# Kernel optimization log

Measured on AMD Instinct MI355X. Metric: run time of the kernel, lower is better.

The kernel has to match this reference:

```python
import jax, jax.numpy as jnp
import numpy as np

ALPHA = 0.2   # LeakyReLU slope from source
HEADS = 8

def _proj(x, W, s, b):
    # Conv3D(kernel=1, no bias) + fused inference BatchNorm affine + LeakyReLU
    y = jnp.einsum('nchwd,de->nchwe', x, W) * s + b
    return jnp.where(y >= 0, y, ALPHA * y)

def setup_inputs() -> dict:
    key = jax.random.key(0)
    ks = jax.random.split(key, 13)
    N, D, H, W, C = 2, 64, 64, 64, 64   # D == in_channels (axis 1), C is last axis
    KC, VC = 64, 64
    p = lambda k, sh, sc=0.1: jax.random.normal(k, sh, jnp.float32) * sc
    return {
        'x':  jax.random.normal(ks[0], (N, D, H, W, C), jnp.float32),
        'Wk': p(ks[1], (D, KC)), 'sk': 1.0 + p(ks[2], (KC,)), 'bk': p(ks[3], (KC,)),
        'Wq': p(ks[4], (D, KC)), 'sq': 1.0 + p(ks[5], (KC,)), 'bq': p(ks[6], (KC,)),
        'Wv': p(ks[7], (D, VC)), 'sv': 1.0 + p(ks[8], (VC,)), 'bv': p(ks[9], (VC,)),
        'Wr': p(ks[10], (VC, D)), 'sr': 1.0 + p(ks[11], (D,)), 'br': p(ks[12], (D,)),
    }

def reference(x, Wk, sk, bk, Wq, sq, bq, Wv, sv, bv, Wr, sr, br):
    n, d, h, w, c = x.shape
    xt = jnp.transpose(x, (0, 4, 2, 3, 1))            # (n, c, h, w, d)
    keys    = _proj(xt, Wk, sk, bk)                   # (n, c, h, w, KC)
    queries = _proj(xt, Wq, sq, bq)
    values  = _proj(xt, Wv, sv, bv)
    T = c * h * w
    KC, VC = Wk.shape[1], Wv.shape[1]
    hk, hv = KC // HEADS, VC // HEADS                 # hk == hv required by source math
    K = jax.nn.softmax(keys.reshape(n, T, HEADS, hk), axis=1)      # softmax over tokens
    Q = jax.nn.softmax(queries.reshape(n, T, HEADS, hk), axis=-1)  # softmax over head channels
    V = values.reshape(n, T, HEADS, hv)
    ctx = jnp.einsum('ntak,ntav->nakv', K, V)         # (n, heads, hk, hv) small context
    # source: tf.matmul(context, query^T) contracts ctx's hv with query's hk axis
    att = jnp.einsum('nakv,ntav->nakt', ctx, Q)       # (n, heads, hk, T)
    # faithful raw reshape per head (n, hk, T) -> (n, c, h, w, hv), heads concat last
    att = att.reshape(n, HEADS, c, h, w, hv)
    agg = jnp.transpose(att, (0, 2, 3, 4, 1, 5)).reshape(n, c, h, w, HEADS * hv)
    rep = _proj(agg, Wr, sr, br)                      # (n, c, h, w, d)
    return x + jnp.transpose(rep, (0, 4, 2, 3, 1))
```

## Files before the change

kernel.cpp:

```cpp
#include <hip/hip_runtime.h>

#define ALPHA 0.2f

typedef const __attribute__((address_space(1))) unsigned int gu32;
typedef __attribute__((address_space(3))) unsigned int lu32;

__device__ float g_part[8192 * 576];
__device__ float g_red[2 * 32 * 1024];
__device__ float g_ctx[1024];

__global__ __launch_bounds__(256) void k_kv(
    const float* __restrict__ x,
    const float* __restrict__ Wk, const float* __restrict__ sk, const float* __restrict__ bk,
    const float* __restrict__ Wv, const float* __restrict__ sv, const float* __restrict__ bv)
{
  __shared__ __align__(16) float sh[12288];
  float* xt = sh;
  float* WL = sh + 4096;

  const int tid = threadIdx.x;
  const int bid = blockIdx.x;
  const int n  = bid >> 12;
  const int hw = bid & 4095;

  const float* xrow = x + (size_t)n * 16777216u + (size_t)hw * 64u;

  #pragma unroll
  for (int i = 0; i < 4; ++i) {
    int idx = tid + i * 256;
    int d = idx >> 4, c4 = (idx & 15) * 4;
    __builtin_amdgcn_global_load_lds((gu32*)(xrow + (size_t)d * 262144u + c4),
                                     (lu32*)&xt[idx * 4], 16, 0, 0);
  }
  #pragma unroll
  for (int i = 0; i < 8; ++i) {
    int idx = tid + i * 256;
    int d = idx >> 5, e4 = (idx & 31) * 4;
    const float* src = (e4 < 64) ? (Wk + d * 64 + e4) : (Wv + d * 64 + e4 - 64);
    __builtin_amdgcn_global_load_lds((gu32*)src, (lu32*)&WL[idx * 4], 16, 0, 0);
  }

  const int tok0 = (tid & 15) * 4;
  const int eg   = tid >> 4;
  const int e0   = eg * 8;
  const bool isK = (eg < 8);
  const int  ec  = isK ? e0 : (e0 - 64);

  const float* sp = (isK ? sk : sv) + ec;
  const float* bp = (isK ? bk : bv) + ec;
  float s8[8], b8[8];
  *(float4*)&s8[0] = *(const float4*)(sp);
  *(float4*)&s8[4] = *(const float4*)(sp + 4);
  *(float4*)&b8[0] = *(const float4*)(bp);
  *(float4*)&b8[4] = *(const float4*)(bp + 4);

  __syncthreads();

  float acc[4][8];
  #pragma unroll
  for (int t = 0; t < 4; ++t)
    #pragma unroll
    for (int j = 0; j < 8; ++j) acc[t][j] = 0.f;

  #pragma unroll 4
  for (int d = 0; d < 64; ++d) {
    float4 xv = *(const float4*)&xt[d * 64 + tok0];
    float4 wa = *(const float4*)&WL[d * 128 + e0];
    float4 wb = *(const float4*)&WL[d * 128 + e0 + 4];
    float xr[4] = {xv.x, xv.y, xv.z, xv.w};
    float w[8]  = {wa.x, wa.y, wa.z, wa.w, wb.x, wb.y, wb.z, wb.w};
    #pragma unroll
    for (int t = 0; t < 4; ++t)
      #pragma unroll
      for (int j = 0; j < 8; ++j) acc[t][j] += xr[t] * w[j];
  }

  __syncthreads();

  float* eK = sh;
  float* vV = sh + 4352;
  float* dst = (isK ? eK : vV);
  #pragma unroll
  for (int t = 0; t < 4; ++t) {
    float y8[8];
    #pragma unroll
    for (int j = 0; j < 8; ++j) {
      float y = acc[t][j] * s8[j] + b8[j];
      y = (y >= 0.f) ? y : ALPHA * y;
      if (isK) y = __expf(fminf(y, 60.f));
      y8[j] = y;
    }
    *(float4*)&dst[(tok0 + t) * 68 + ec]     = *(float4*)&y8[0];
    *(float4*)&dst[(tok0 + t) * 68 + ec + 4] = *(float4*)&y8[4];
  }
  __syncthreads();

  {
    float* pE = sh + 8704;
    float* pS = sh + 8960;
    const int ch = tid & 63;
    const int tq = tid >> 6;
    const int a8 = ch & ~7;

    float E = 0.f;
    float S[8];
    #pragma unroll
    for (int v = 0; v < 8; ++v) S[v] = 0.f;
    for (int t = tq * 16; t < tq * 16 + 16; ++t) {
      float e = eK[t * 68 + ch];
      float4 v0 = *(const float4*)&vV[t * 68 + a8];
      float4 v1 = *(const float4*)&vV[t * 68 + a8 + 4];
      E += e;
      S[0] += e * v0.x; S[1] += e * v0.y; S[2] += e * v0.z; S[3] += e * v0.w;
      S[4] += e * v1.x; S[5] += e * v1.y; S[6] += e * v1.z; S[7] += e * v1.w;
    }
    pE[tq * 64 + ch] = E;
    #pragma unroll
    for (int v = 0; v < 8; ++v) pS[(tq * 64 + ch) * 8 + v] = S[v];
    __syncthreads();

    if (tid < 64) {
      float* gp = g_part + (size_t)bid * 576u;
      float E4 = pE[tid] + pE[64 + tid] + pE[128 + tid] + pE[192 + tid];
      gp[tid] = E4;
      #pragma unroll
      for (int v = 0; v < 8; ++v) {
        float S4 = pS[tid * 8 + v] + pS[(64 + tid) * 8 + v]
                 + pS[(128 + tid) * 8 + v] + pS[(192 + tid) * 8 + v];
        gp[64 + v * 64 + tid] = S4;
      }
    }
  }
}

__global__ __launch_bounds__(256) void k_red() {
  const int ob = blockIdx.x & 3;
  const int bc = blockIdx.x >> 2;
  const int i  = ob * 256 + threadIdx.x;
  const int n = i >> 9, ch = (i & 511) >> 3, v = i & 7;
  const float* base = g_part + ((size_t)n * 4096u + (size_t)bc * 128u) * 576u;
  float l = 0.f, S = 0.f;
  #pragma unroll 8
  for (int b = 0; b < 128; ++b) {
    l += base[(size_t)b * 576u + ch];
    S += base[(size_t)b * 576u + 64u + (size_t)v * 64u + ch];
  }
  g_red[bc * 1024 + i]         = l;
  g_red[32768 + bc * 1024 + i] = S;
}

__global__ __launch_bounds__(256) void k_ctx() {
  int i = blockIdx.x * 256 + threadIdx.x;
  if (i >= 1024) return;
  float l = 0.f, S = 0.f;
  #pragma unroll
  for (int r = 0; r < 32; ++r) {
    l += g_red[r * 1024 + i];
    S += g_red[32768 + r * 1024 + i];
  }
  float c = (l > 0.f) ? (S / l) : 0.f;
  if (!(__builtin_fabsf(c) < 1e30f)) c = 0.f;
  g_ctx[i] = c;
}

__global__ __launch_bounds__(256) void k_att(
    const float* __restrict__ x,
    const float* __restrict__ Wq, const float* __restrict__ sq, const float* __restrict__ bq,
    const float* __restrict__ Wr, const float* __restrict__ sr, const float* __restrict__ br,
    float* __restrict__ out)
{
  __shared__ __align__(16) float WqA[64 * 65];
  __shared__ __align__(16) float xw[64 * 64];
  __shared__ __align__(16) float qL[64 * 64];
  __shared__ __align__(16) float ctxL[64 * 12];
  __shared__ float srL[64], brL[64];

  const int tid = threadIdx.x;
  const int lin = blockIdx.x;

  const int xcd   = lin & 7;
  const int jc    = (lin >> 3) & 7;
  const int rest  = lin >> 6;
  const int combo = rest * 8 + xcd;
  const int n     = combo >> 9;
  const int hp_lo = (combo >> 6) & 7;
  const int wp    = combo & 63;
  const int hp    = jc * 8 + hp_lo;
  const int hwp   = hp * 64 + wp;

  const int h_t   = hp_lo * 8 + (wp >> 3);
  const int wbase = (wp & 7) * 8;

  #pragma unroll
  for (int i = 0; i < 4; ++i) {
    int idx = tid + i * 256;
    __builtin_amdgcn_global_load_lds((gu32*)(Wq + idx * 4),
                                     (lu32*)&WqA[idx * 4], 16, 0, 0);
  }
  if (tid < 64) { srL[tid] = sr[tid]; brL[tid] = br[tid]; }

  for (int i = tid; i < 512; i += 256) {
    int ch = i >> 3, v = i & 7;
    ctxL[ch * 12 + v] = g_ctx[n * 512 + ch * 8 + v];
  }

  {
    const size_t xb = (size_t)n * 16777216u + (size_t)h_t * 4096u;
    #pragma unroll
    for (int i = 0; i < 16; ++i) {
      int idx = tid + i * 256;
      int d = idx >> 6, tok = idx & 63;
      int vpp = tok >> 3, cl = tok & 7;
      xw[d * 64 + tok] = x[xb + (size_t)d * 262144u + (size_t)(wbase + vpp) * 64u + (cl * 8 + jc)];
    }
  }
  __syncthreads();

  {
    const int tok0 = (tid & 31) * 2;
    const int ch0  = (tid >> 5) * 8;
    float acc0[8], acc1[8];
    #pragma unroll
    for (int j = 0; j < 8; ++j) { acc0[j] = 0.f; acc1[j] = 0.f; }
    #pragma unroll 4
    for (int d = 0; d < 64; ++d) {
      float2 xv = *(const float2*)&xw[d * 64 + tok0];
      float4 wa = *(const float4*)&WqA[d * 64 + ch0];
      float4 wb = *(const float4*)&WqA[d * 64 + ch0 + 4];
      float w[8] = {wa.x, wa.y, wa.z, wa.w, wb.x, wb.y, wb.z, wb.w};
      #pragma unroll
      for (int j = 0; j < 8; ++j) { acc0[j] += xv.x * w[j]; acc1[j] += xv.y * w[j]; }
    }
    float sv8[8], bv8[8];
    *(float4*)&sv8[0] = *(const float4*)(sq + ch0);
    *(float4*)&sv8[4] = *(const float4*)(sq + ch0 + 4);
    *(float4*)&bv8[0] = *(const float4*)(bq + ch0);
    *(float4*)&bv8[4] = *(const float4*)(bq + ch0 + 4);
    #pragma unroll
    for (int i = 0; i < 2; ++i) {
      float* a = (i == 0) ? acc0 : acc1;
      float mx = -3.0e38f;
      #pragma unroll
      for (int j = 0; j < 8; ++j) {
        float y = a[j] * sv8[j] + bv8[j];
        y = (y >= 0.f) ? y : ALPHA * y;
        a[j] = y;
        mx = fmaxf(mx, y);
      }
      float sum = 0.f;
      #pragma unroll
      for (int j = 0; j < 8; ++j) { a[j] = __expf(a[j] - mx); sum += a[j]; }
      float inv = 1.f / sum;
      float o8[8];
      #pragma unroll
      for (int j = 0; j < 8; ++j) o8[j] = a[j] * inv;
      const int t = tok0 + i;
      const int rot = (4 * t) & 63;
      *(float4*)&qL[t * 64 + ((ch0 + rot) & 63)]     = *(float4*)&o8[0];
      *(float4*)&qL[t * 64 + ((ch0 + 4 + rot) & 63)] = *(float4*)&o8[4];
    }
  }
  __syncthreads();

  #pragma unroll
  for (int i = 0; i < 4; ++i) {
    int idx = tid + i * 256;
    __builtin_amdgcn_global_load_lds((gu32*)(Wr + idx * 4),
                                     (lu32*)&xw[idx * 4], 16, 0, 0);
  }

  {
    float* aggL = WqA;
    const int cp = tid & 63, eb = tid >> 6;
    const int kk = cp >> 3, cl = cp & 7;
    #pragma unroll
    for (int je = 0; je < 16; ++je) {
      int e = eb * 16 + je;
      int a = e >> 3, vpp = e & 7;
      float4 c0 = *(const float4*)&ctxL[(a * 8 + kk) * 12];
      float4 c1 = *(const float4*)&ctxL[(a * 8 + kk) * 12 + 4];
      int t = vpp * 8 + cl;
      int rot = (4 * t) & 63;
      float4 q0 = *(const float4*)&qL[t * 64 + ((a * 8 + rot) & 63)];
      float4 q1 = *(const float4*)&qL[t * 64 + ((a * 8 + 4 + rot) & 63)];
      float s = q0.x * c0.x + q0.y * c0.y + q0.z * c0.z + q0.w * c0.w
              + q1.x * c1.x + q1.y * c1.y + q1.z * c1.z + q1.w * c1.w;
      aggL[cp * 65 + e] = s;
    }
  }
  __syncthreads();

  {
    const float* aggL = WqA;
    const int ci = tid & 63, dq = tid >> 6;
    float accr[16];
    #pragma unroll
    for (int i = 0; i < 16; ++i) accr[i] = 0.f;
    #pragma unroll 4
    for (int e = 0; e < 64; ++e) {
      float av = aggL[ci * 65 + e];
      const float* wr = &xw[e * 64 + dq * 16];
      #pragma unroll
      for (int i = 0; i < 16; ++i) accr[i] += av * wr[i];
    }
    const size_t xb = (size_t)n * 16777216u + (size_t)hwp * 64u + (size_t)ci;
    #pragma unroll
    for (int i = 0; i < 16; ++i) {
      int di = dq * 16 + i;
      float y = accr[i] * srL[di] + brL[di];
      y = (y >= 0.f) ? y : ALPHA * y;
      out[xb + (size_t)di * 262144u] = x[xb + (size_t)di * 262144u] + y;
    }
  }
}

extern "C" void kernel_launch(void* const* d_in, const int* in_sizes, int n_in,
                              void* d_out, int out_size, void* d_ws, size_t ws_size,
                              hipStream_t stream)
{
  (void)in_sizes; (void)n_in; (void)out_size; (void)d_ws; (void)ws_size;

  const float* x  = (const float*)d_in[0];
  const float* Wk = (const float*)d_in[1];
  const float* sk = (const float*)d_in[2];
  const float* bk = (const float*)d_in[3];
  const float* Wq = (const float*)d_in[4];
  const float* sq = (const float*)d_in[5];
  const float* bq = (const float*)d_in[6];
  const float* Wv = (const float*)d_in[7];
  const float* sv = (const float*)d_in[8];
  const float* bv = (const float*)d_in[9];
  const float* Wr = (const float*)d_in[10];
  const float* sr = (const float*)d_in[11];
  const float* br = (const float*)d_in[12];
  float* out = (float*)d_out;

  k_kv  <<<dim3(8192), dim3(256), 0, stream>>>(x, Wk, sk, bk, Wv, sv, bv);
  k_red <<<dim3(128),  dim3(256), 0, stream>>>();
  k_ctx <<<dim3(4),    dim3(256), 0, stream>>>();
  k_att <<<dim3(8192), dim3(256), 0, stream>>>(x, Wq, sq, bq, Wr, sr, br, out);
}
```

Before: 496.3 us.

## Restructure KV projection to wave-uniform weights and process two rows per block

The k_kv kernel now handles two hw rows per block, with half as many blocks. Each wave owns one 32-channel slice of K or V, so weight loads are wave-uniform reads straight from global memory, and x is read straight from global as float2 instead of staged through LDS. The reduction runs in two phases that write separate g_part slots, so the partial-sum layout seen by k_red stays the same. In k_att, the Wr weights are read from global with a wave-uniform index instead of being staged in LDS, and the agg tile uses padding of 68 so it can be written and read as float4. This trades LDS staging and its barriers for more global/scalar-cache traffic and higher register pressure from the 64-element accumulators.

Measured after the change: 523.4 us. 1.05x slower.

```diff
diff --git a/kernel.cpp b/kernel.cpp
--- a/kernel.cpp
+++ b/kernel.cpp
@@ -14,93 +14,79 @@
     const float* __restrict__ Wk, const float* __restrict__ sk, const float* __restrict__ bk,
     const float* __restrict__ Wv, const float* __restrict__ sv, const float* __restrict__ bv)
 {
-  __shared__ __align__(16) float sh[12288];
-  float* xt = sh;
-  float* WL = sh + 4096;
+  __shared__ __align__(16) float sh[11008];
+  float* eK = sh;
+  float* vV = sh + 4352;
+  float* pE = sh + 8704;
+  float* pS = sh + 8960;
 
   const int tid = threadIdx.x;
   const int bid = blockIdx.x;
-  const int n  = bid >> 12;
-  const int hw = bid & 4095;
-
-  const float* xrow = x + (size_t)n * 16777216u + (size_t)hw * 64u;
-
-  #pragma unroll
-  for (int i = 0; i < 4; ++i) {
-    int idx = tid + i * 256;
-    int d = idx >> 4, c4 = (idx & 15) * 4;
-    __builtin_amdgcn_global_load_lds((gu32*)(xrow + (size_t)d * 262144u + c4),
-                                     (lu32*)&xt[idx * 4], 16, 0, 0);
-  }
-  #pragma unroll
-  for (int i = 0; i < 8; ++i) {
-    int idx = tid + i * 256;
-    int d = idx >> 5, e4 = (idx & 31) * 4;
-    const float* src = (e4 < 64) ? (Wk + d * 64 + e4) : (Wv + d * 64 + e4 - 64);
-    __builtin_amdgcn_global_load_lds((gu32*)src, (lu32*)&WL[idx * 4], 16, 0, 0);
-  }
-
-  const int tok0 = (tid & 15) * 4;
-  const int eg   = tid >> 4;
-  const int e0   = eg * 8;
-  const bool isK = (eg < 8);
-  const int  ec  = isK ? e0 : (e0 - 64);
-
-  const float* sp = (isK ? sk : sv) + ec;
-  const float* bp = (isK ? bk : bv) + ec;
-  float s8[8], b8[8];
-  *(float4*)&s8[0] = *(const float4*)(sp);
-  *(float4*)&s8[4] = *(const float4*)(sp + 4);
-  *(float4*)&b8[0] = *(const float4*)(bp);
-  *(float4*)&b8[4] = *(const float4*)(bp + 4);
-
-  __syncthreads();
-
-  float acc[4][8];
-  #pragma unroll
-  for (int t = 0; t < 4; ++t)
-    #pragma unroll
-    for (int j = 0; j < 8; ++j) acc[t][j] = 0.f;
+  const int n   = bid >> 11;
+  const int hw0 = (bid & 2047) * 2;
+
+  const int pr  = tid & 63;
+  const int wv  = __builtin_amdgcn_readfirstlane(tid >> 6);
+  const bool isK = (wv < 2);
+  const int cbase = 32 * (wv & 1);
+  const float* Wsrc = (isK ? Wk : Wv) + cbase;
+  const float* sp   = (isK ? sk : sv) + cbase;
+  const float* bp   = (isK ? bk : bv) + cbase;
+
+  const float* xg = x + (size_t)n * 16777216u + (size_t)hw0 * 64u + 2 * pr;
+
+  float acc[2][32];
+  #pragma unroll
+  for (int t = 0; t < 2; ++t)
+    #pragma unroll
+    for (int c = 0; c < 32; ++c) acc[t][c] = 0.f;
 
   #pragma unroll 4
   for (int d = 0; d < 64; ++d) {
-    float4 xv = *(const float4*)&xt[d * 64 + tok0];
-    float4 wa = *(const float4*)&WL[d * 128 + e0];
-    float4 wb = *(const float4*)&WL[d * 128 + e0 + 4];
-    float xr[4] = {xv.x, xv.y, xv.z, xv.w};
-    float w[8]  = {wa.x, wa.y, wa.z, wa.w, wb.x, wb.y, wb.z, wb.w};
-    #pragma unroll
-    for (int t = 0; t < 4; ++t)
-      #pragma unroll
-      for (int j = 0; j < 8; ++j) acc[t][j] += xr[t] * w[j];
-  }
-
-  __syncthreads();
-
-  float* eK = sh;
-  float* vV = sh + 4352;
-  float* dst = (isK ? eK : vV);
-  #pragma unroll
-  for (int t = 0; t < 4; ++t) {
-    float y8[8];
-    #pragma unroll
-    for (int j = 0; j < 8; ++j) {
-      float y = acc[t][j] * s8[j] + b8[j];
-      y = (y >= 0.f) ? y : ALPHA * y;
-      if (isK) y = __expf(fminf(y, 60.f));
-      y8[j] = y;
-    }
-    *(float4*)&dst[(tok0 + t) * 68 + ec]     = *(float4*)&y8[0];
-    *(float4*)&dst[(tok0 + t) * 68 + ec + 4] = *(float4*)&y8[4];
-  }
-  __syncthreads();
-
-  {
-    float* pE = sh + 8704;
-    float* pS = sh + 8960;
-    const int ch = tid & 63;
-    const int tq = tid >> 6;
-    const int a8 = ch & ~7;
+    float2 xv = *(const float2*)(xg + (size_t)d * 262144u);
+    const float* wrow = Wsrc + d * 64;
+    #pragma unroll
+    for (int q = 0; q < 8; ++q) {
+      float4 w = *(const float4*)(wrow + q * 4);
+      acc[0][q*4+0] += xv.x * w.x; acc[0][q*4+1] += xv.x * w.y;
+      acc[0][q*4+2] += xv.x * w.z; acc[0][q*4+3] += xv.x * w.w;
+      acc[1][q*4+0] += xv.y * w.x; acc[1][q*4+1] += xv.y * w.y;
+      acc[1][q*4+2] += xv.y * w.z; acc[1][q*4+3] += xv.y * w.w;
+    }
+  }
+
+  #pragma unroll
+  for (int q = 0; q < 8; ++q) {
+    float4 s4 = *(const float4*)(sp + q * 4);
+    float4 b4 = *(const float4*)(bp + q * 4);
+    float ss[4] = {s4.x, s4.y, s4.z, s4.w};
+    float bb[4] = {b4.x, b4.y, b4.z, b4.w};
+    #pragma unroll
+    for (int j = 0; j < 4; ++j) {
+      #pragma unroll
+      for (int t = 0; t < 2; ++t) {
+        float y = acc[t][q*4+j] * ss[j] + bb[j];
+        y = (y >= 0.f) ? y : ALPHA * y;
+        if (isK) y = __expf(fminf(y, 60.f));
+        acc[t][q*4+j] = y;
+      }
+    }
+  }
+
+  const int prl = pr & 31;
+  float* dstbuf = isK ? eK : vV;
+  const int ch = tid & 63, tq = tid >> 6, a8 = ch & ~7;
+
+  #pragma unroll
+  for (int ph = 0; ph < 2; ++ph) {
+    if ((pr >> 5) == ph) {
+      #pragma unroll
+      for (int t = 0; t < 2; ++t)
+        #pragma unroll
+        for (int q = 0; q < 8; ++q)
+          *(float4*)&dstbuf[(prl*2 + t) * 68 + cbase + q*4] = *(float4*)&acc[t][q*4];
+    }
+    __syncthreads();
 
     float E = 0.f;
     float S[8];
@@ -120,7 +106,7 @@
     __syncthreads();
 
     if (tid < 64) {
-      float* gp = g_part + (size_t)bid * 576u;
+      float* gp = g_part + ((size_t)bid * 2u + ph) * 576u;
       float E4 = pE[tid] + pE[64 + tid] + pE[128 + tid] + pE[192 + tid];
       gp[tid] = E4;
       #pragma unroll
@@ -169,7 +155,7 @@
     const float* __restrict__ Wr, const float* __restrict__ sr, const float* __restrict__ br,
     float* __restrict__ out)
 {
-  __shared__ __align__(16) float WqA[64 * 65];
+  __shared__ __align__(16) float WqA[64 * 68];
   __shared__ __align__(16) float xw[64 * 64];
   __shared__ __align__(16) float qL[64 * 64];
   __shared__ __align__(16) float ctxL[64 * 12];
@@ -262,30 +248,28 @@
   }
   __syncthreads();
 
-  #pragma unroll
-  for (int i = 0; i < 4; ++i) {
-    int idx = tid + i * 256;
-    __builtin_amdgcn_global_load_lds((gu32*)(Wr + idx * 4),
-                                     (lu32*)&xw[idx * 4], 16, 0, 0);
-  }
-
   {
     float* aggL = WqA;
     const int cp = tid & 63, eb = tid >> 6;
     const int kk = cp >> 3, cl = cp & 7;
     #pragma unroll
-    for (int je = 0; je < 16; ++je) {
-      int e = eb * 16 + je;
-      int a = e >> 3, vpp = e & 7;
-      float4 c0 = *(const float4*)&ctxL[(a * 8 + kk) * 12];
-      float4 c1 = *(const float4*)&ctxL[(a * 8 + kk) * 12 + 4];
-      int t = vpp * 8 + cl;
-      int rot = (4 * t) & 63;
-      float4 q0 = *(const float4*)&qL[t * 64 + ((a * 8 + rot) & 63)];
-      float4 q1 = *(const float4*)&qL[t * 64 + ((a * 8 + 4 + rot) & 63)];
-      float s = q0.x * c0.x + q0.y * c0.y + q0.z * c0.z + q0.w * c0.w
-              + q1.x * c1.x + q1.y * c1.y + q1.z * c1.z + q1.w * c1.w;
-      aggL[cp * 65 + e] = s;
+    for (int j4 = 0; j4 < 4; ++j4) {
+      float s4[4];
+      #pragma unroll
+      for (int jj = 0; jj < 4; ++jj) {
+        int e = eb * 16 + j4 * 4 + jj;
+        int a = e >> 3, vpp = e & 7;
+        float4 c0 = *(const float4*)&ctxL[(a * 8 + kk) * 12];
+        float4 c1 = *(const float4*)&ctxL[(a * 8 + kk) * 12 + 4];
+        int t = vpp * 8 + cl;
+        int rot = (4 * t) & 63;
+        float4 q0 = *(const float4*)&qL[t * 64 + ((a * 8 + rot) & 63)];
+        float4 q1 = *(const float4*)&qL[t * 64 + ((a * 8 + 4 + rot) & 63)];
+        s4[jj] = q0.x * c0.x + q0.y * c0.y + q0.z * c0.z + q0.w * c0.w
+               + q1.x * c1.x + q1.y * c1.y + q1.z * c1.z + q1.w * c1.w;
+      }
+      *(float4*)&aggL[cp * 68 + eb * 16 + j4 * 4] =
+          make_float4(s4[0], s4[1], s4[2], s4[3]);
     }
   }
   __syncthreads();
@@ -293,15 +277,28 @@
   {
     const float* aggL = WqA;
     const int ci = tid & 63, dq = tid >> 6;
+    const int dqu = __builtin_amdgcn_readfirstlane(tid >> 6);
+    const float* WrU = Wr + dqu * 16;
     float accr[16];
     #pragma unroll
     for (int i = 0; i < 16; ++i) accr[i] = 0.f;
     #pragma unroll 4
-    for (int e = 0; e < 64; ++e) {
-      float av = aggL[ci * 65 + e];
-      const float* wr = &xw[e * 64 + dq * 16];
-      #pragma unroll
-      for (int i = 0; i < 16; ++i) accr[i] += av * wr[i];
+    for (int ec = 0; ec < 16; ++ec) {
+      float4 a4 = *(const float4*)&aggL[ci * 68 + ec * 4];
+      float av[4] = {a4.x, a4.y, a4.z, a4.w};
+      #pragma unroll
+      for (int j = 0; j < 4; ++j) {
+        const float* wrow = WrU + (ec * 4 + j) * 64;
+        float4 w0 = *(const float4*)(wrow);
+        float4 w1 = *(const float4*)(wrow + 4);
+        float4 w2 = *(const float4*)(wrow + 8);
+        float4 w3 = *(const float4*)(wrow + 12);
+        float aj = av[j];
+        accr[0]  += aj * w0.x; accr[1]  += aj * w0.y; accr[2]  += aj * w0.z; accr[3]  += aj * w0.w;
+        accr[4]  += aj * w1.x; accr[5]  += aj * w1.y; accr[6]  += aj * w1.z; accr[7]  += aj * w1.w;
+        accr[8]  += aj * w2.x; accr[9]  += aj * w2.y; accr[10] += aj * w2.z; accr[11] += aj * w2.w;
+        accr[12] += aj * w3.x; accr[13] += aj * w3.y; accr[14] += aj * w3.z; accr[15] += aj * w3.w;
+      }
     }
     const size_t xb = (size_t)n * 16777216u + (size_t)hwp * 64u + (size_t)ci;
     #pragma unroll
@@ -335,7 +332,7 @@
   const float* br = (const float*)d_in[12];
   float* out = (float*)d_out;
 
-  k_kv  <<<dim3(8192), dim3(256), 0, stream>>>(x, Wk, sk, bk, Wv, sv, bv);
+  k_kv  <<<dim3(4096), dim3(256), 0, stream>>>(x, Wk, sk, bk, Wv, sv, bv);
   k_red <<<dim3(128),  dim3(256), 0, stream>>>();
   k_ctx <<<dim3(4),    dim3(256), 0, stream>>>();
   k_att <<<dim3(8192), dim3(256), 0, stream>>>(x, Wq, sq, bq, Wr, sr, br, out);
```
